# Kernel optimization log

Measured on AMD Instinct MI355X. Metric: run time of the kernel, lower is better.

## Reference

```python
import jax, jax.numpy as jnp
import numpy as np

N = 100000
E = 600000
D_IN, D_HID, D_OUT = 128, 128, 64


def setup_inputs() -> dict:
    key = jax.random.key(0)
    k1, k2, k3, k4 = jax.random.split(key, 4)
    x = jax.random.normal(k1, (N, D_IN), dtype=jnp.float32)
    edge_index = jax.random.randint(k2, (2, E), 0, N, dtype=jnp.int64)
    edge_weight = jnp.ones((E,), dtype=jnp.float32)
    W1 = jax.random.normal(k3, (D_IN, D_HID), dtype=jnp.float32) / np.sqrt(D_IN)
    b1 = jnp.zeros((D_HID,), dtype=jnp.float32)
    W2 = jax.random.normal(k4, (D_HID, D_OUT), dtype=jnp.float32) / np.sqrt(D_HID)
    b2 = jnp.zeros((D_OUT,), dtype=jnp.float32)
    return {"x": x, "edge_index": edge_index, "edge_weight": edge_weight,
            "W1": W1, "b1": b1, "W2": W2, "b2": b2}


def _gcn_conv(x, row, col, ew, W, b, n_nodes):
    # x: [N, d_in]; row/col/ew include self loops. PyG gcn_norm:
    # deg[i] = sum of ew over edges with target i; norm = d^-1/2[row]*ew*d^-1/2[col]
    deg = jax.ops.segment_sum(ew, col, num_segments=n_nodes)
    dinv = jnp.where(deg > 0, jax.lax.rsqrt(deg), 0.0)
    norm = dinv[row] * ew * dinv[col]  # [E+N]
    xw = x @ W  # dense transform first (d_out <= d_in path)
    msg = xw[row] * norm[:, None]  # gather + scale  [E+N, d_out]
    out = jax.ops.segment_sum(msg, col, num_segments=n_nodes)  # scatter-add
    return out + b


def reference(x, edge_index, edge_weight, W1, b1, W2, b2):
    n = x.shape[0]
    loops = jnp.arange(n, dtype=edge_index.dtype)
    row = jnp.concatenate([edge_index[0], loops])
    col = jnp.concatenate([edge_index[1], loops])
    ew = jnp.concatenate([edge_weight, jnp.ones((n,), dtype=edge_weight.dtype)])
    # dropout is identity in eval mode
    h = jax.nn.relu(_gcn_conv(x, row, col, ew, W1, b1, n))
    out = _gcn_conv(h, row, col, ew, W2, b2, n)
    return out
```

## Files before the change

kernel.cpp:

```cpp
#include <hip/hip_runtime.h>


constexpr int SCAN_BLOCKS = 256;

typedef __attribute__((ext_vector_type(8))) short short8;
typedef __attribute__((ext_vector_type(4))) float f32x4;

__device__ __forceinline__ ushort f2bf(float f) {
    unsigned u = __float_as_uint(f);
    return (ushort)((u + 0x7fffu + ((u >> 16) & 1u)) >> 16);
}
__device__ __forceinline__ float bf2f(ushort h) {
    return __uint_as_float((unsigned)h << 16);
}

__global__ void cnt_kernel(const int* __restrict__ col, int* __restrict__ cnt,
                           int* __restrict__ rank, int E) {
    const int stride = gridDim.x * blockDim.x;
    for (int e = blockIdx.x * blockDim.x + threadIdx.x; e < E; e += stride)
        rank[e] = atomicAdd(&cnt[col[e]], 1);
}

__global__ __launch_bounds__(256) void scan_part_kernel(
        const int* __restrict__ cnt, int* __restrict__ partial, int N) {
    const int T = SCAN_BLOCKS * 256;
    const int chunk = (N + T - 1) / T;
    const int j = blockIdx.x * 256 + threadIdx.x;
    const int s = j * chunk, e = min(s + chunk, N);
    int acc = 0;
    for (int i = s; i < e; i++) acc += cnt[i];
    __shared__ int red[256];
    red[threadIdx.x] = acc;
    __syncthreads();
    for (int off = 128; off > 0; off >>= 1) {
        if (threadIdx.x < off) red[threadIdx.x] += red[threadIdx.x + off];
        __syncthreads();
    }
    if (threadIdx.x == 0) partial[blockIdx.x] = red[0];
}

__global__ __launch_bounds__(256) void scan_tops_kernel(int* __restrict__ partial) {
    __shared__ int sh[256];
    const int t = threadIdx.x;
    int v = (t < SCAN_BLOCKS) ? partial[t] : 0;
    sh[t] = v;
    __syncthreads();
    for (int off = 1; off < 256; off <<= 1) {
        int x = sh[t];
        int a = (t >= off) ? sh[t - off] : 0;
        __syncthreads();
        sh[t] = x + a;
        __syncthreads();
    }
    if (t < SCAN_BLOCKS) partial[t] = (t == 0) ? 0 : sh[t - 1];
}

__global__ __launch_bounds__(256) void scan_write_kernel(
        const int* __restrict__ cnt, const int* __restrict__ partial,
        int* __restrict__ rowptr, int N) {
    const int T = SCAN_BLOCKS * 256;
    const int chunk = (N + T - 1) / T;
    const int j = blockIdx.x * 256 + threadIdx.x;
    const int s = j * chunk, e = min(s + chunk, N);
    int acc = 0;
    for (int i = s; i < e; i++) acc += cnt[i];
    __shared__ int sh[256];
    const int t = threadIdx.x;
    sh[t] = acc;
    __syncthreads();
    for (int off = 1; off < 256; off <<= 1) {
        int x = sh[t];
        int a = (t >= off) ? sh[t - off] : 0;
        __syncthreads();
        sh[t] = x + a;
        __syncthreads();
    }
    int excl = partial[blockIdx.x] + ((t == 0) ? 0 : sh[t - 1]);
    for (int i = s; i < e; i++) {
        rowptr[i] = excl;
        excl += cnt[i];
    }
    if (j == T - 1) rowptr[N] = excl;
}

__global__ void fill_kernel(const int* __restrict__ row, const int* __restrict__ col,
        const float* __restrict__ ew, const int* __restrict__ rowptr,
        const int* __restrict__ rank, int2* __restrict__ csr, int E) {
    int e = blockIdx.x * blockDim.x + threadIdx.x;
    if (e < E) {
        const int p = rowptr[col[e]] + rank[e];
        csr[p] = make_int2(row[e], __float_as_int(ew[e]));
    }
}

__global__ __launch_bounds__(256) void degsum_kernel(
        const int* __restrict__ rowptr, const int2* __restrict__ csr,
        float* __restrict__ dinv, int N) {
    const int n = blockIdx.x * blockDim.x + threadIdx.x;
    if (n >= N) return;
    const int e0 = rowptr[n], e1 = rowptr[n + 1];
    float d = 1.0f;
    for (int e = e0; e < e1; e++) d += __int_as_float(csr[e].y);
    dinv[n] = (d > 0.0f) ? rsqrtf(d) : 0.0f;
}

__global__ __launch_bounds__(256) void misc_kernel(
        int2* __restrict__ csr, const float* __restrict__ dinv, int E,
        const float* __restrict__ X, ushort* __restrict__ Xb, int nx4,
        const float* __restrict__ W1, ushort* __restrict__ W1t,
        const float* __restrict__ W2, ushort* __restrict__ W2t) {
    const int nb_x = (nx4 + 255) / 256;
    const int nb_p = (E + 255) / 256;
    int b = blockIdx.x;
    if (b < nb_x) {
        const int i = b * 256 + threadIdx.x;
        if (i < nx4) {
            float4 v = reinterpret_cast<const float4*>(X)[i];
            ushort4 o;
            o.x = f2bf(v.x); o.y = f2bf(v.y); o.z = f2bf(v.z); o.w = f2bf(v.w);
            reinterpret_cast<ushort4*>(Xb)[i] = o;
        }
        return;
    }
    b -= nb_x;
    if (b < nb_p) {
        const int e = b * 256 + threadIdx.x;
        if (e < E) {
            int2 c = csr[e];
            ((float*)csr)[2 * (size_t)e + 1] = __int_as_float(c.y) * dinv[c.x];
        }
        return;
    }
    b -= nb_p;
    if (b < 64) {
        const int o = b * 256 + threadIdx.x;
        W1t[o] = f2bf(W1[(size_t)(o & 127) * 128 + (o >> 7)]);
        return;
    }
    b -= 64;
    {
        const int o = b * 256 + threadIdx.x;
        if (o < 64 * 128)
            W2t[o] = f2bf(W2[(size_t)(o & 127) * 64 + (o >> 7)]);
    }
}

template <int DOUT, bool OUT_BF16>
__global__ __launch_bounds__(256, 2) void mfma_gemm_kernel(
        const ushort* __restrict__ Xb, const ushort* __restrict__ Wt,
        void* __restrict__ Y, int N) {
    constexpr int CW = DOUT / 64;
    constexpr int RW = 4 / CW;
    constexpr int WROWS = 128 / RW;
    constexpr int MI = WROWS / 16;
    __shared__ __align__(16) ushort sX[128 * 128];
    __shared__ __align__(16) ushort sW[DOUT * 128];
    const int tid = threadIdx.x;
    const int base = blockIdx.x * 128;

    #pragma unroll
    for (int p = 0; p < 8; p++) {
        const int ch = p * 256 + tid;
        const int r = ch >> 4, cpos = ch & 15;
        const int grow = base + r;
        uint4 v = make_uint4(0, 0, 0, 0);
        if (grow < N)
            v = *reinterpret_cast<const uint4*>(Xb + (size_t)grow * 128 + cpos * 8);
        const int b = (cpos * 16) ^ ((r & 7) << 4);
        *reinterpret_cast<uint4*>(reinterpret_cast<char*>(sX) + r * 256 + b) = v;
    }
    for (int ch = tid; ch < DOUT * 16; ch += 256) {
        const int r = ch >> 4, cpos = ch & 15;
        uint4 v = *reinterpret_cast<const uint4*>(Wt + (size_t)r * 128 + cpos * 8);
        const int b = (cpos * 16) ^ ((r & 7) << 4);
        *reinterpret_cast<uint4*>(reinterpret_cast<char*>(sW) + r * 256 + b) = v;
    }
    __syncthreads();

    const int lane = tid & 63;
    const int wid = tid >> 6;
    const int wr = wid / CW;
    const int wc = wid % CW;
    const int lr = lane & 15;
    const int g  = lane >> 4;

    f32x4 acc[MI][4];
    #pragma unroll
    for (int i = 0; i < MI; i++)
        #pragma unroll
        for (int f = 0; f < 4; f++)
            acc[i][f] = (f32x4){0.f, 0.f, 0.f, 0.f};

    #pragma unroll
    for (int ks = 0; ks < 4; ks++) {
        const int koff = ks * 64 + g * 16;
        short8 a[MI], b[4];
        #pragma unroll
        for (int i = 0; i < MI; i++) {
            const int row = wr * WROWS + i * 16 + lr;
            a[i] = *reinterpret_cast<const short8*>(
                reinterpret_cast<const char*>(sX) + row * 256 + (koff ^ ((row & 7) << 4)));
        }
        #pragma unroll
        for (int f = 0; f < 4; f++) {
            const int col = wc * 64 + f * 16 + lr;
            b[f] = *reinterpret_cast<const short8*>(
                reinterpret_cast<const char*>(sW) + col * 256 + (koff ^ ((col & 7) << 4)));
        }
        #pragma unroll
        for (int i = 0; i < MI; i++)
            #pragma unroll
            for (int f = 0; f < 4; f++)
                acc[i][f] = __builtin_amdgcn_mfma_f32_16x16x32_bf16(a[i], b[f], acc[i][f], 0, 0, 0);
    }

    #pragma unroll
    for (int i = 0; i < MI; i++) {
        #pragma unroll
        for (int reg = 0; reg < 4; reg++) {
            const int grow = base + wr * WROWS + i * 16 + g * 4 + reg;
            if (grow < N) {
                #pragma unroll
                for (int f = 0; f < 4; f++) {
                    const int gcol = wc * 64 + f * 16 + lr;
                    const float v = acc[i][f][reg];
                    if (OUT_BF16)
                        ((ushort*)Y)[(size_t)grow * DOUT + gcol] = f2bf(v);
                    else
                        ((float*)Y)[(size_t)grow * DOUT + gcol] = v;
                }
            }
        }
    }
}

__global__ __launch_bounds__(256) void agg1_kernel(
        const int* __restrict__ rowptr, const int2* __restrict__ csr,
        const float* __restrict__ dinv,
        const ushort* __restrict__ src, const float* __restrict__ bias,
        ushort* __restrict__ dst, int N) {
    const long long gid = (long long)blockIdx.x * blockDim.x + threadIdx.x;
    const int c = (int)(gid >> 5);
    if (c >= N) return;
    const int lane = (int)(gid & 31);
    const float di = dinv[c];
    const float sl = di * di;
    ushort4 s4 = *reinterpret_cast<const ushort4*>(src + (size_t)c * 128 + lane * 4);
    float ax = bf2f(s4.x) * sl, ay = bf2f(s4.y) * sl,
          az = bf2f(s4.z) * sl, aw = bf2f(s4.w) * sl;
    const int e0 = rowptr[c], e1 = rowptr[c + 1];
    int e = e0;
    for (; e + 4 <= e1; e += 4) {
        const int2 c0 = csr[e], c1 = csr[e + 1], c2 = csr[e + 2], c3 = csr[e + 3];
        const ushort4 v0 = *reinterpret_cast<const ushort4*>(src + (size_t)c0.x * 128 + lane * 4);
        const ushort4 v1 = *reinterpret_cast<const ushort4*>(src + (size_t)c1.x * 128 + lane * 4);
        const ushort4 v2 = *reinterpret_cast<const ushort4*>(src + (size_t)c2.x * 128 + lane * 4);
        const ushort4 v3 = *reinterpret_cast<const ushort4*>(src + (size_t)c3.x * 128 + lane * 4);
        const float w0 = __int_as_float(c0.y) * di;
        const float w1 = __int_as_float(c1.y) * di;
        const float w2 = __int_as_float(c2.y) * di;
        const float w3 = __int_as_float(c3.y) * di;
        ax += bf2f(v0.x) * w0 + bf2f(v1.x) * w1 + bf2f(v2.x) * w2 + bf2f(v3.x) * w3;
        ay += bf2f(v0.y) * w0 + bf2f(v1.y) * w1 + bf2f(v2.y) * w2 + bf2f(v3.y) * w3;
        az += bf2f(v0.z) * w0 + bf2f(v1.z) * w1 + bf2f(v2.z) * w2 + bf2f(v3.z) * w3;
        aw += bf2f(v0.w) * w0 + bf2f(v1.w) * w1 + bf2f(v2.w) * w2 + bf2f(v3.w) * w3;
    }
    for (; e < e1; e++) {
        const int2 ce = csr[e];
        const float w = __int_as_float(ce.y) * di;
        const ushort4 v4 = *reinterpret_cast<const ushort4*>(src + (size_t)ce.x * 128 + lane * 4);
        ax += bf2f(v4.x) * w; ay += bf2f(v4.y) * w;
        az += bf2f(v4.z) * w; aw += bf2f(v4.w) * w;
    }
    const float4 b = reinterpret_cast<const float4*>(bias)[lane];
    ax = fmaxf(ax + b.x, 0.f); ay = fmaxf(ay + b.y, 0.f);
    az = fmaxf(az + b.z, 0.f); aw = fmaxf(aw + b.w, 0.f);
    ushort4 o;
    o.x = f2bf(ax); o.y = f2bf(ay); o.z = f2bf(az); o.w = f2bf(aw);
    *reinterpret_cast<ushort4*>(dst + (size_t)c * 128 + lane * 4) = o;
}

__global__ __launch_bounds__(256) void agg2_kernel(
        const int* __restrict__ rowptr, const int2* __restrict__ csr,
        const float* __restrict__ dinv,
        const ushort* __restrict__ src, const float* __restrict__ bias,
        float* __restrict__ dst, int N) {
    const long long gid = (long long)blockIdx.x * blockDim.x + threadIdx.x;
    const int c = (int)(gid >> 4);
    if (c >= N) return;
    const int lane = (int)(gid & 15);
    const float di = dinv[c];
    const float sl = di * di;
    ushort4 s4 = *reinterpret_cast<const ushort4*>(src + (size_t)c * 64 + lane * 4);
    float ax = bf2f(s4.x) * sl, ay = bf2f(s4.y) * sl,
          az = bf2f(s4.z) * sl, aw = bf2f(s4.w) * sl;
    const int e0 = rowptr[c], e1 = rowptr[c + 1];
    int e = e0;
    for (; e + 4 <= e1; e += 4) {
        const int2 c0 = csr[e], c1 = csr[e + 1], c2 = csr[e + 2], c3 = csr[e + 3];
        const ushort4 v0 = *reinterpret_cast<const ushort4*>(src + (size_t)c0.x * 64 + lane * 4);
        const ushort4 v1 = *reinterpret_cast<const ushort4*>(src + (size_t)c1.x * 64 + lane * 4);
        const ushort4 v2 = *reinterpret_cast<const ushort4*>(src + (size_t)c2.x * 64 + lane * 4);
        const ushort4 v3 = *reinterpret_cast<const ushort4*>(src + (size_t)c3.x * 64 + lane * 4);
        const float w0 = __int_as_float(c0.y) * di;
        const float w1 = __int_as_float(c1.y) * di;
        const float w2 = __int_as_float(c2.y) * di;
        const float w3 = __int_as_float(c3.y) * di;
        ax += bf2f(v0.x) * w0 + bf2f(v1.x) * w1 + bf2f(v2.x) * w2 + bf2f(v3.x) * w3;
        ay += bf2f(v0.y) * w0 + bf2f(v1.y) * w1 + bf2f(v2.y) * w2 + bf2f(v3.y) * w3;
        az += bf2f(v0.z) * w0 + bf2f(v1.z) * w1 + bf2f(v2.z) * w2 + bf2f(v3.z) * w3;
        aw += bf2f(v0.w) * w0 + bf2f(v1.w) * w1 + bf2f(v2.w) * w2 + bf2f(v3.w) * w3;
    }
    for (; e < e1; e++) {
        const int2 ce = csr[e];
        const float w = __int_as_float(ce.y) * di;
        const ushort4 v4 = *reinterpret_cast<const ushort4*>(src + (size_t)ce.x * 64 + lane * 4);
        ax += bf2f(v4.x) * w; ay += bf2f(v4.y) * w;
        az += bf2f(v4.z) * w; aw += bf2f(v4.w) * w;
    }
    const float4 b = reinterpret_cast<const float4*>(bias)[lane];
    float4 o = make_float4(ax + b.x, ay + b.y, az + b.z, aw + b.w);
    reinterpret_cast<float4*>(dst)[(size_t)c * 16 + lane] = o;
}

extern "C" void kernel_launch(void* const* d_in, const int* in_sizes, int n_in,
                              void* d_out, int out_size, void* d_ws, size_t ws_size,
                              hipStream_t stream) {
    const float* x  = (const float*)d_in[0];
    const int*   ei = (const int*)d_in[1];
    const float* ew = (const float*)d_in[2];
    const float* W1 = (const float*)d_in[3];
    const float* b1 = (const float*)d_in[4];
    const float* W2 = (const float*)d_in[5];
    const float* b2 = (const float*)d_in[6];
    const int N = in_sizes[0] / 128;
    const int E = in_sizes[1] / 2;
    const int* row = ei;
    const int* col = ei + E;

    char* w = (char*)d_ws;
    float* dinv = (float*)w;                 w += (size_t)N * 4;
    ushort* Xb  = (ushort*)w;
    ushort* Gb  = (ushort*)w;
                                             w += (size_t)N * 256;
    ushort* Ab  = (ushort*)w;                w += (size_t)N * 256;
    ushort* Hb  = (ushort*)w;                w += (size_t)N * 256;
    ushort* W1t = (ushort*)w;                w += 128 * 128 * 2;
    ushort* W2t = (ushort*)w;                w += 64 * 128 * 2;
    int* cnt    = (int*)w;                   w += (size_t)N * 4;
    int* rowptr = (int*)w;                   w += (size_t)(N + 1) * 4;
    int* partial= (int*)w;                   w += SCAN_BLOCKS * 4;
    int* rank   = (int*)w;                   w += (size_t)E * 4;
    int2* csr   = (int2*)w;
    float* out  = (float*)d_out;

    hipMemsetAsync(cnt, 0, (size_t)N * sizeof(int), stream);

    const int eb4 = (E / 4 + 255) / 256;
    cnt_kernel<<<eb4, 256, 0, stream>>>(col, cnt, rank, E);
    scan_part_kernel<<<SCAN_BLOCKS, 256, 0, stream>>>(cnt, partial, N);
    scan_tops_kernel<<<1, 256, 0, stream>>>(partial);
    scan_write_kernel<<<SCAN_BLOCKS, 256, 0, stream>>>(cnt, partial, rowptr, N);
    fill_kernel<<<(E + 255) / 256, 256, 0, stream>>>(row, col, ew, rowptr, rank, csr, E);
    degsum_kernel<<<(N + 255) / 256, 256, 0, stream>>>(rowptr, csr, dinv, N);

    const int nx4 = N * 32;
    const int misc_blocks = (nx4 + 255) / 256 + (E + 255) / 256 + 64 + 32;
    misc_kernel<<<misc_blocks, 256, 0, stream>>>(csr, dinv, E, x, Xb, nx4,
                                                 W1, W1t, W2, W2t);

    const int ntiles = (N + 127) / 128;

    mfma_gemm_kernel<128, true><<<ntiles, 256, 0, stream>>>(Xb, W1t, Ab, N);
    agg1_kernel<<<(int)(((long long)N * 32 + 255) / 256), 256, 0, stream>>>(
        rowptr, csr, dinv, Ab, b1, Hb, N);

    mfma_gemm_kernel<64, true><<<ntiles, 256, 0, stream>>>(Hb, W2t, Gb, N);
    agg2_kernel<<<(int)(((long long)N * 16 + 255) / 256), 256, 0, stream>>>(
        rowptr, csr, dinv, Gb, b2, out, N);
}
```

Before: 161.3 us.

## Fuse X conversion into GEMM1, overlap edge counting, merge scan stages, widen aggregation

GEMM1 now reads fp32 X and converts it to bf16 while staging into shared memory, so the separate Xb pass is gone. Extra blocks in the same launch perform the atomic edge counting, overlapping that work with the GEMM. The memset is replaced by a prep kernel that also transposes the weights. The scan-tops kernel is folded into scan_write, and the per-edge dinv pre-scaling pass is dropped in favour of looking up dinv[src] inside the aggregation kernels. Aggregation now uses 16-byte loads with 8 features per thread, at the cost of an extra dependent gather per edge.

```diff
diff --git a/kernel.cpp b/kernel.cpp
--- a/kernel.cpp
+++ b/kernel.cpp
@@ -14,11 +14,123 @@
     return __uint_as_float((unsigned)h << 16);
 }
 
-__global__ void cnt_kernel(const int* __restrict__ col, int* __restrict__ cnt,
-                           int* __restrict__ rank, int E) {
-    const int stride = gridDim.x * blockDim.x;
-    for (int e = blockIdx.x * blockDim.x + threadIdx.x; e < E; e += stride)
-        rank[e] = atomicAdd(&cnt[col[e]], 1);
+__global__ __launch_bounds__(256) void prep_kernel(
+        int* __restrict__ cnt, int N,
+        const float* __restrict__ W1, ushort* __restrict__ W1t,
+        const float* __restrict__ W2, ushort* __restrict__ W2t) {
+    const int n4c = (N + 3) >> 2;
+    const int nbz = (n4c + 255) / 256;
+    int b = blockIdx.x;
+    if (b < nbz) {
+        const int i = b * 256 + threadIdx.x;
+        if (i < n4c) reinterpret_cast<int4*>(cnt)[i] = make_int4(0, 0, 0, 0);
+        return;
+    }
+    b -= nbz;
+    if (b < 64) {
+        const int o = b * 256 + threadIdx.x;
+        W1t[o] = f2bf(W1[(size_t)(o & 127) * 128 + (o >> 7)]);
+        return;
+    }
+    b -= 64;
+    {
+        const int o = b * 256 + threadIdx.x;
+        if (o < 64 * 128)
+            W2t[o] = f2bf(W2[(size_t)(o & 127) * 64 + (o >> 7)]);
+    }
+}
+
+__global__ __launch_bounds__(256, 2) void combo1_kernel(
+        const float* __restrict__ X, const ushort* __restrict__ W1t,
+        ushort* __restrict__ Ab, int N, int G,
+        const int* __restrict__ col, int* __restrict__ cnt,
+        int* __restrict__ rank, int E) {
+    __shared__ __align__(16) ushort sX[128 * 128];
+    __shared__ __align__(16) ushort sW[128 * 128];
+    const int tid = threadIdx.x;
+
+    if (blockIdx.x >= G) {
+        const int T = (gridDim.x - G) * 256;
+        for (int e = (blockIdx.x - G) * 256 + tid; e < E; e += T)
+            rank[e] = atomicAdd(&cnt[col[e]], 1);
+        return;
+    }
+
+    const int base = blockIdx.x * 128;
+    #pragma unroll
+    for (int p = 0; p < 8; p++) {
+        const int ch = p * 256 + tid;
+        const int r = ch >> 4, cpos = ch & 15;
+        const int grow = base + r;
+        uint4 u = make_uint4(0, 0, 0, 0);
+        if (grow < N) {
+            const float* xp = X + (size_t)grow * 128 + cpos * 8;
+            const float4 a = *reinterpret_cast<const float4*>(xp);
+            const float4 c = *reinterpret_cast<const float4*>(xp + 4);
+            u.x = (uint)f2bf(a.x) | ((uint)f2bf(a.y) << 16);
+            u.y = (uint)f2bf(a.z) | ((uint)f2bf(a.w) << 16);
+            u.z = (uint)f2bf(c.x) | ((uint)f2bf(c.y) << 16);
+            u.w = (uint)f2bf(c.z) | ((uint)f2bf(c.w) << 16);
+        }
+        const int b = (cpos * 16) ^ ((r & 7) << 4);
+        *reinterpret_cast<uint4*>(reinterpret_cast<char*>(sX) + r * 256 + b) = u;
+    }
+    #pragma unroll
+    for (int p = 0; p < 8; p++) {
+        const int ch = p * 256 + tid;
+        const int r = ch >> 4, cpos = ch & 15;
+        uint4 v = *reinterpret_cast<const uint4*>(W1t + (size_t)r * 128 + cpos * 8);
+        const int b = (cpos * 16) ^ ((r & 7) << 4);
+        *reinterpret_cast<uint4*>(reinterpret_cast<char*>(sW) + r * 256 + b) = v;
+    }
+    __syncthreads();
+
+    const int lane = tid & 63;
+    const int wid = tid >> 6;
+    const int wr = wid >> 1;
+    const int wc = wid & 1;
+    const int lr = lane & 15;
+    const int g  = lane >> 4;
+
+    f32x4 acc[4][4];
+    #pragma unroll
+    for (int i = 0; i < 4; i++)
+        #pragma unroll
+        for (int f = 0; f < 4; f++) acc[i][f] = (f32x4){0.f, 0.f, 0.f, 0.f};
+
+    #pragma unroll
+    for (int ks = 0; ks < 4; ks++) {
+        const int koff = ks * 64 + g * 16;
+        short8 a[4], b[4];
+        #pragma unroll
+        for (int i = 0; i < 4; i++) {
+            const int row = wr * 64 + i * 16 + lr;
+            a[i] = *reinterpret_cast<const short8*>(
+                reinterpret_cast<const char*>(sX) + row * 256 + (koff ^ ((row & 7) << 4)));
+        }
+        #pragma unroll
+        for (int f = 0; f < 4; f++) {
+            const int c = wc * 64 + f * 16 + lr;
+            b[f] = *reinterpret_cast<const short8*>(
+                reinterpret_cast<const char*>(sW) + c * 256 + (koff ^ ((c & 7) << 4)));
+        }
+        #pragma unroll
+        for (int i = 0; i < 4; i++)
+            #pragma unroll
+            for (int f = 0; f < 4; f++)
+                acc[i][f] = __builtin_amdgcn_mfma_f32_16x16x32_bf16(a[i], b[f], acc[i][f], 0, 0, 0);
+    }
+
+    #pragma unroll
+    for (int i = 0; i < 4; i++)
+        #pragma unroll
+        for (int reg = 0; reg < 4; reg++) {
+            const int grow = base + wr * 64 + i * 16 + g * 4 + reg;
+            if (grow < N)
+                #pragma unroll
+                for (int f = 0; f < 4; f++)
+                    Ab[(size_t)grow * 128 + wc * 64 + f * 16 + lr] = f2bf(acc[i][f][reg]);
+        }
 }
 
 __global__ __launch_bounds__(256) void scan_part_kernel(
@@ -39,33 +151,29 @@
     if (threadIdx.x == 0) partial[blockIdx.x] = red[0];
 }
 
-__global__ __launch_bounds__(256) void scan_tops_kernel(int* __restrict__ partial) {
-    __shared__ int sh[256];
-    const int t = threadIdx.x;
-    int v = (t < SCAN_BLOCKS) ? partial[t] : 0;
-    sh[t] = v;
-    __syncthreads();
-    for (int off = 1; off < 256; off <<= 1) {
-        int x = sh[t];
-        int a = (t >= off) ? sh[t - off] : 0;
-        __syncthreads();
-        sh[t] = x + a;
-        __syncthreads();
-    }
-    if (t < SCAN_BLOCKS) partial[t] = (t == 0) ? 0 : sh[t - 1];
-}
-
 __global__ __launch_bounds__(256) void scan_write_kernel(
         const int* __restrict__ cnt, const int* __restrict__ partial,
         int* __restrict__ rowptr, int N) {
+    __shared__ int tp[256];
+    __shared__ int sh[256];
+    const int t = threadIdx.x;
+    tp[t] = partial[t];
+    __syncthreads();
+    for (int off = 1; off < 256; off <<= 1) {
+        int x = tp[t];
+        int a = (t >= off) ? tp[t - off] : 0;
+        __syncthreads();
+        tp[t] = x + a;
+        __syncthreads();
+    }
+    const int blockOff = (blockIdx.x == 0) ? 0 : tp[blockIdx.x - 1];
+
     const int T = SCAN_BLOCKS * 256;
     const int chunk = (N + T - 1) / T;
-    const int j = blockIdx.x * 256 + threadIdx.x;
+    const int j = blockIdx.x * 256 + t;
     const int s = j * chunk, e = min(s + chunk, N);
     int acc = 0;
     for (int i = s; i < e; i++) acc += cnt[i];
-    __shared__ int sh[256];
-    const int t = threadIdx.x;
     sh[t] = acc;
     __syncthreads();
     for (int off = 1; off < 256; off <<= 1) {
@@ -75,7 +183,7 @@
         sh[t] = x + a;
         __syncthreads();
     }
-    int excl = partial[blockIdx.x] + ((t == 0) ? 0 : sh[t - 1]);
+    int excl = blockOff + ((t == 0) ? 0 : sh[t - 1]);
     for (int i = s; i < e; i++) {
         rowptr[i] = excl;
         excl += cnt[i];
@@ -104,57 +212,116 @@
     dinv[n] = (d > 0.0f) ? rsqrtf(d) : 0.0f;
 }
 
-__global__ __launch_bounds__(256) void misc_kernel(
-        int2* __restrict__ csr, const float* __restrict__ dinv, int E,
-        const float* __restrict__ X, ushort* __restrict__ Xb, int nx4,
-        const float* __restrict__ W1, ushort* __restrict__ W1t,
-        const float* __restrict__ W2, ushort* __restrict__ W2t) {
-    const int nb_x = (nx4 + 255) / 256;
-    const int nb_p = (E + 255) / 256;
-    int b = blockIdx.x;
-    if (b < nb_x) {
-        const int i = b * 256 + threadIdx.x;
-        if (i < nx4) {
-            float4 v = reinterpret_cast<const float4*>(X)[i];
-            ushort4 o;
-            o.x = f2bf(v.x); o.y = f2bf(v.y); o.z = f2bf(v.z); o.w = f2bf(v.w);
-            reinterpret_cast<ushort4*>(Xb)[i] = o;
-        }
-        return;
-    }
-    b -= nb_x;
-    if (b < nb_p) {
-        const int e = b * 256 + threadIdx.x;
-        if (e < E) {
-            int2 c = csr[e];
-            ((float*)csr)[2 * (size_t)e + 1] = __int_as_float(c.y) * dinv[c.x];
-        }
-        return;
-    }
-    b -= nb_p;
-    if (b < 64) {
-        const int o = b * 256 + threadIdx.x;
-        W1t[o] = f2bf(W1[(size_t)(o & 127) * 128 + (o >> 7)]);
-        return;
-    }
-    b -= 64;
+__global__ __launch_bounds__(256) void agg1_kernel(
+        const int* __restrict__ rowptr, const int2* __restrict__ csr,
+        const float* __restrict__ dinv,
+        const ushort* __restrict__ src, const float* __restrict__ bias,
+        ushort* __restrict__ dst, int N) {
+    const long long gid = (long long)blockIdx.x * blockDim.x + threadIdx.x;
+    const int c = (int)(gid >> 4);
+    if (c >= N) return;
+    const int lane = (int)(gid & 15);
+    const float di = dinv[c];
+    const float sl = di * di;
+    float acc[8];
     {
-        const int o = b * 256 + threadIdx.x;
-        if (o < 64 * 128)
-            W2t[o] = f2bf(W2[(size_t)(o & 127) * 64 + (o >> 7)]);
-    }
-}
-
-template <int DOUT, bool OUT_BF16>
-__global__ __launch_bounds__(256, 2) void mfma_gemm_kernel(
+        const short8 s8 = *reinterpret_cast<const short8*>(src + (size_t)c * 128 + lane * 8);
+        #pragma unroll
+        for (int j = 0; j < 8; j++) acc[j] = bf2f((ushort)s8[j]) * sl;
+    }
+    const int e0 = rowptr[c], e1 = rowptr[c + 1];
+    int e = e0;
+    for (; e + 4 <= e1; e += 4) {
+        const int2 c0 = csr[e], c1 = csr[e + 1], c2 = csr[e + 2], c3 = csr[e + 3];
+        const float w0 = __int_as_float(c0.y) * dinv[c0.x] * di;
+        const float w1 = __int_as_float(c1.y) * dinv[c1.x] * di;
+        const float w2 = __int_as_float(c2.y) * dinv[c2.x] * di;
+        const float w3 = __int_as_float(c3.y) * dinv[c3.x] * di;
+        const short8 v0 = *reinterpret_cast<const short8*>(src + (size_t)c0.x * 128 + lane * 8);
+        const short8 v1 = *reinterpret_cast<const short8*>(src + (size_t)c1.x * 128 + lane * 8);
+        const short8 v2 = *reinterpret_cast<const short8*>(src + (size_t)c2.x * 128 + lane * 8);
+        const short8 v3 = *reinterpret_cast<const short8*>(src + (size_t)c3.x * 128 + lane * 8);
+        #pragma unroll
+        for (int j = 0; j < 8; j++)
+            acc[j] += bf2f((ushort)v0[j]) * w0 + bf2f((ushort)v1[j]) * w1 +
+                      bf2f((ushort)v2[j]) * w2 + bf2f((ushort)v3[j]) * w3;
+    }
+    for (; e < e1; e++) {
+        const int2 ce = csr[e];
+        const float w = __int_as_float(ce.y) * dinv[ce.x] * di;
+        const short8 v = *reinterpret_cast<const short8*>(src + (size_t)ce.x * 128 + lane * 8);
+        #pragma unroll
+        for (int j = 0; j < 8; j++) acc[j] += bf2f((ushort)v[j]) * w;
+    }
+    const float4 b0 = reinterpret_cast<const float4*>(bias)[lane * 2];
+    const float4 b1 = reinterpret_cast<const float4*>(bias)[lane * 2 + 1];
+    acc[0] = fmaxf(acc[0] + b0.x, 0.f); acc[1] = fmaxf(acc[1] + b0.y, 0.f);
+    acc[2] = fmaxf(acc[2] + b0.z, 0.f); acc[3] = fmaxf(acc[3] + b0.w, 0.f);
+    acc[4] = fmaxf(acc[4] + b1.x, 0.f); acc[5] = fmaxf(acc[5] + b1.y, 0.f);
+    acc[6] = fmaxf(acc[6] + b1.z, 0.f); acc[7] = fmaxf(acc[7] + b1.w, 0.f);
+    uint4 o;
+    o.x = (uint)f2bf(acc[0]) | ((uint)f2bf(acc[1]) << 16);
+    o.y = (uint)f2bf(acc[2]) | ((uint)f2bf(acc[3]) << 16);
+    o.z = (uint)f2bf(acc[4]) | ((uint)f2bf(acc[5]) << 16);
+    o.w = (uint)f2bf(acc[6]) | ((uint)f2bf(acc[7]) << 16);
+    *reinterpret_cast<uint4*>(dst + (size_t)c * 128 + lane * 8) = o;
+}
+
+__global__ __launch_bounds__(256) void agg2_kernel(
+        const int* __restrict__ rowptr, const int2* __restrict__ csr,
+        const float* __restrict__ dinv,
+        const ushort* __restrict__ src, const float* __restrict__ bias,
+        float* __restrict__ dst, int N) {
+    const long long gid = (long long)blockIdx.x * blockDim.x + threadIdx.x;
+    const int c = (int)(gid >> 3);
+    if (c >= N) return;
+    const int lane = (int)(gid & 7);
+    const float di = dinv[c];
+    const float sl = di * di;
+    float acc[8];
+    {
+        const short8 s8 = *reinterpret_cast<const short8*>(src + (size_t)c * 64 + lane * 8);
+        #pragma unroll
+        for (int j = 0; j < 8; j++) acc[j] = bf2f((ushort)s8[j]) * sl;
+    }
+    const int e0 = rowptr[c], e1 = rowptr[c + 1];
+    int e = e0;
+    for (; e + 4 <= e1; e += 4) {
+        const int2 c0 = csr[e], c1 = csr[e + 1], c2 = csr[e + 2], c3 = csr[e + 3];
+        const float w0 = __int_as_float(c0.y) * dinv[c0.x] * di;
+        const float w1 = __int_as_float(c1.y) * dinv[c1.x] * di;
+        const float w2 = __int_as_float(c2.y) * dinv[c2.x] * di;
+        const float w3 = __int_as_float(c3.y) * dinv[c3.x] * di;
+        const short8 v0 = *reinterpret_cast<const short8*>(src + (size_t)c0.x * 64 + lane * 8);
+        const short8 v1 = *reinterpret_cast<const short8*>(src + (size_t)c1.x * 64 + lane * 8);
+        const short8 v2 = *reinterpret_cast<const short8*>(src + (size_t)c2.x * 64 + lane * 8);
+        const short8 v3 = *reinterpret_cast<const short8*>(src + (size_t)c3.x * 64 + lane * 8);
+        #pragma unroll
+        for (int j = 0; j < 8; j++)
+            acc[j] += bf2f((ushort)v0[j]) * w0 + bf2f((ushort)v1[j]) * w1 +
+                      bf2f((ushort)v2[j]) * w2 + bf2f((ushort)v3[j]) * w3;
+    }
+    for (; e < e1; e++) {
+        const int2 ce = csr[e];
+        const float w = __int_as_float(ce.y) * dinv[ce.x] * di;
+        const short8 v = *reinterpret_cast<const short8*>(src + (size_t)ce.x * 64 + lane * 8);
+        #pragma unroll
+        for (int j = 0; j < 8; j++) acc[j] += bf2f((ushort)v[j]) * w;
+    }
+    const float4 b0 = reinterpret_cast<const float4*>(bias)[lane * 2];
+    const float4 b1 = reinterpret_cast<const float4*>(bias)[lane * 2 + 1];
+    float* dp = dst + (size_t)c * 64 + lane * 8;
+    *reinterpret_cast<float4*>(dp) =
+        make_float4(acc[0] + b0.x, acc[1] + b0.y, acc[2] + b0.z, acc[3] + b0.w);
+    *reinterpret_cast<float4*>(dp + 4) =
+        make_float4(acc[4] + b1.x, acc[5] + b1.y, acc[6] + b1.z, acc[7] + b1.w);
+}
+
+__global__ __launch_bounds__(256, 2) void gemm2_kernel(
         const ushort* __restrict__ Xb, const ushort* __restrict__ Wt,
-        void* __restrict__ Y, int N) {
-    constexpr int CW = DOUT / 64;
-    constexpr int RW = 4 / CW;
-    constexpr int WROWS = 128 / RW;
-    constexpr int MI = WROWS / 16;
+        ushort* __restrict__ Y, int N) {
     __shared__ __align__(16) ushort sX[128 * 128];
-    __shared__ __align__(16) ushort sW[DOUT * 128];
+    __shared__ __align__(16) ushort sW[64 * 128];
     const int tid = threadIdx.x;
     const int base = blockIdx.x * 128;
 
@@ -169,7 +336,9 @@
         const int b = (cpos * 16) ^ ((r & 7) << 4);
         *reinterpret_cast<uint4*>(reinterpret_cast<char*>(sX) + r * 256 + b) = v;
     }
-    for (int ch = tid; ch < DOUT * 16; ch += 256) {
+    #pragma unroll
+    for (int p = 0; p < 4; p++) {
+        const int ch = p * 256 + tid;
         const int r = ch >> 4, cpos = ch & 15;
         uint4 v = *reinterpret_cast<const uint4*>(Wt + (size_t)r * 128 + cpos * 8);
         const int b = (cpos * 16) ^ ((r & 7) << 4);
@@ -179,148 +348,48 @@
 
     const int lane = tid & 63;
     const int wid = tid >> 6;
-    const int wr = wid / CW;
-    const int wc = wid % CW;
     const int lr = lane & 15;
     const int g  = lane >> 4;
 
-    f32x4 acc[MI][4];
-    #pragma unroll
-    for (int i = 0; i < MI; i++)
-        #pragma unroll
-        for (int f = 0; f < 4; f++)
-            acc[i][f] = (f32x4){0.f, 0.f, 0.f, 0.f};
+    f32x4 acc[2][4];
+    #pragma unroll
+    for (int i = 0; i < 2; i++)
+        #pragma unroll
+        for (int f = 0; f < 4; f++) acc[i][f] = (f32x4){0.f, 0.f, 0.f, 0.f};
 
     #pragma unroll
     for (int ks = 0; ks < 4; ks++) {
         const int koff = ks * 64 + g * 16;
-        short8 a[MI], b[4];
-        #pragma unroll
-        for (int i = 0; i < MI; i++) {
-            const int row = wr * WROWS + i * 16 + lr;
+        short8 a[2], b[4];
+        #pragma unroll
+        for (int i = 0; i < 2; i++) {
+            const int row = wid * 32 + i * 16 + lr;
             a[i] = *reinterpret_cast<const short8*>(
                 reinterpret_cast<const char*>(sX) + row * 256 + (koff ^ ((row & 7) << 4)));
         }
         #pragma unroll
         for (int f = 0; f < 4; f++) {
-            const int col = wc * 64 + f * 16 + lr;
+            const int c = f * 16 + lr;
             b[f] = *reinterpret_cast<const short8*>(
-                reinterpret_cast<const char*>(sW) + col * 256 + (koff ^ ((col & 7) << 4)));
-        }
-        #pragma unroll
-        for (int i = 0; i < MI; i++)
+                reinterpret_cast<const char*>(sW) + c * 256 + (koff ^ ((c & 7) << 4)));
+        }
+        #pragma unroll
+        for (int i = 0; i < 2; i++)
             #pragma unroll
             for (int f = 0; f < 4; f++)
                 acc[i][f] = __builtin_amdgcn_mfma_f32_16x16x32_bf16(a[i], b[f], acc[i][f], 0, 0, 0);
     }
 
     #pragma unroll
-    for (int i = 0; i < MI; i++) {
+    for (int i = 0; i < 2; i++)
         #pragma unroll
         for (int reg = 0; reg < 4; reg++) {
-            const int grow = base + wr * WROWS + i * 16 + g * 4 + reg;
-            if (grow < N) {
+            const int grow = base + wid * 32 + i * 16 + g * 4 + reg;
+            if (grow < N)
                 #pragma unroll
-                for (int f = 0; f < 4; f++) {
-                    const int gcol = wc * 64 + f * 16 + lr;
-                    const float v = acc[i][f][reg];
-                    if (OUT_BF16)
-                        ((ushort*)Y)[(size_t)grow * DOUT + gcol] = f2bf(v);
-                    else
-                        ((float*)Y)[(size_t)grow * DOUT + gcol] = v;
-                }
-            }
-        }
-    }
-}
-
-__global__ __launch_bounds__(256) void agg1_kernel(
-        const int* __restrict__ rowptr, const int2* __restrict__ csr,
-        const float* __restrict__ dinv,
-        const ushort* __restrict__ src, const float* __restrict__ bias,
-        ushort* __restrict__ dst, int N) {
-    const long long gid = (long long)blockIdx.x * blockDim.x + threadIdx.x;
-    const int c = (int)(gid >> 5);
-    if (c >= N) return;
-    const int lane = (int)(gid & 31);
-    const float di = dinv[c];
-    const float sl = di * di;
-    ushort4 s4 = *reinterpret_cast<const ushort4*>(src + (size_t)c * 128 + lane * 4);
-    float ax = bf2f(s4.x) * sl, ay = bf2f(s4.y) * sl,
-          az = bf2f(s4.z) * sl, aw = bf2f(s4.w) * sl;
-    const int e0 = rowptr[c], e1 = rowptr[c + 1];
-    int e = e0;
-    for (; e + 4 <= e1; e += 4) {
-        const int2 c0 = csr[e], c1 = csr[e + 1], c2 = csr[e + 2], c3 = csr[e + 3];
-        const ushort4 v0 = *reinterpret_cast<const ushort4*>(src + (size_t)c0.x * 128 + lane * 4);
-        const ushort4 v1 = *reinterpret_cast<const ushort4*>(src + (size_t)c1.x * 128 + lane * 4);
-        const ushort4 v2 = *reinterpret_cast<const ushort4*>(src + (size_t)c2.x * 128 + lane * 4);
-        const ushort4 v3 = *reinterpret_cast<const ushort4*>(src + (size_t)c3.x * 128 + lane * 4);
-        const float w0 = __int_as_float(c0.y) * di;
-        const float w1 = __int_as_float(c1.y) * di;
-        const float w2 = __int_as_float(c2.y) * di;
-        const float w3 = __int_as_float(c3.y) * di;
-        ax += bf2f(v0.x) * w0 + bf2f(v1.x) * w1 + bf2f(v2.x) * w2 + bf2f(v3.x) * w3;
-        ay += bf2f(v0.y) * w0 + bf2f(v1.y) * w1 + bf2f(v2.y) * w2 + bf2f(v3.y) * w3;
-        az += bf2f(v0.z) * w0 + bf2f(v1.z) * w1 + bf2f(v2.z) * w2 + bf2f(v3.z) * w3;
-        aw += bf2f(v0.w) * w0 + bf2f(v1.w) * w1 + bf2f(v2.w) * w2 + bf2f(v3.w) * w3;
-    }
-    for (; e < e1; e++) {
-        const int2 ce = csr[e];
-        const float w = __int_as_float(ce.y) * di;
-        const ushort4 v4 = *reinterpret_cast<const ushort4*>(src + (size_t)ce.x * 128 + lane * 4);
-        ax += bf2f(v4.x) * w; ay += bf2f(v4.y) * w;
-        az += bf2f(v4.z) * w; aw += bf2f(v4.w) * w;
-    }
-    const float4 b = reinterpret_cast<const float4*>(bias)[lane];
-    ax = fmaxf(ax + b.x, 0.f); ay = fmaxf(ay + b.y, 0.f);
-    az = fmaxf(az + b.z, 0.f); aw = fmaxf(aw + b.w, 0.f);
-    ushort4 o;
-    o.x = f2bf(ax); o.y = f2bf(ay); o.z = f2bf(az); o.w = f2bf(aw);
-    *reinterpret_cast<ushort4*>(dst + (size_t)c * 128 + lane * 4) = o;
-}
-
-__global__ __launch_bounds__(256) void agg2_kernel(
-        const int* __restrict__ rowptr, const int2* __restrict__ csr,
-        const float* __restrict__ dinv,
-        const ushort* __restrict__ src, const float* __restrict__ bias,
-        float* __restrict__ dst, int N) {
-    const long long gid = (long long)blockIdx.x * blockDim.x + threadIdx.x;
-    const int c = (int)(gid >> 4);
-    if (c >= N) return;
-    const int lane = (int)(gid & 15);
-    const float di = dinv[c];
-    const float sl = di * di;
-    ushort4 s4 = *reinterpret_cast<const ushort4*>(src + (size_t)c * 64 + lane * 4);
-    float ax = bf2f(s4.x) * sl, ay = bf2f(s4.y) * sl,
-          az = bf2f(s4.z) * sl, aw = bf2f(s4.w) * sl;
-    const int e0 = rowptr[c], e1 = rowptr[c + 1];
-    int e = e0;
-    for (; e + 4 <= e1; e += 4) {
-        const int2 c0 = csr[e], c1 = csr[e + 1], c2 = csr[e + 2], c3 = csr[e + 3];
-        const ushort4 v0 = *reinterpret_cast<const ushort4*>(src + (size_t)c0.x * 64 + lane * 4);
-        const ushort4 v1 = *reinterpret_cast<const ushort4*>(src + (size_t)c1.x * 64 + lane * 4);
-        const ushort4 v2 = *reinterpret_cast<const ushort4*>(src + (size_t)c2.x * 64 + lane * 4);
-        const ushort4 v3 = *reinterpret_cast<const ushort4*>(src + (size_t)c3.x * 64 + lane * 4);
-        const float w0 = __int_as_float(c0.y) * di;
-        const float w1 = __int_as_float(c1.y) * di;
-        const float w2 = __int_as_float(c2.y) * di;
-        const float w3 = __int_as_float(c3.y) * di;
-        ax += bf2f(v0.x) * w0 + bf2f(v1.x) * w1 + bf2f(v2.x) * w2 + bf2f(v3.x) * w3;
-        ay += bf2f(v0.y) * w0 + bf2f(v1.y) * w1 + bf2f(v2.y) * w2 + bf2f(v3.y) * w3;
-        az += bf2f(v0.z) * w0 + bf2f(v1.z) * w1 + bf2f(v2.z) * w2 + bf2f(v3.z) * w3;
-        aw += bf2f(v0.w) * w0 + bf2f(v1.w) * w1 + bf2f(v2.w) * w2 + bf2f(v3.w) * w3;
-    }
-    for (; e < e1; e++) {
-        const int2 ce = csr[e];
-        const float w = __int_as_float(ce.y) * di;
-        const ushort4 v4 = *reinterpret_cast<const ushort4*>(src + (size_t)ce.x * 64 + lane * 4);
-        ax += bf2f(v4.x) * w; ay += bf2f(v4.y) * w;
-        az += bf2f(v4.z) * w; aw += bf2f(v4.w) * w;
-    }
-    const float4 b = reinterpret_cast<const float4*>(bias)[lane];
-    float4 o = make_float4(ax + b.x, ay + b.y, az + b.z, aw + b.w);
-    reinterpret_cast<float4*>(dst)[(size_t)c * 16 + lane] = o;
+                for (int f = 0; f < 4; f++)
+                    Y[(size_t)grow * 64 + f * 16 + lr] = f2bf(acc[i][f][reg]);
+        }
 }
 
 extern "C" void kernel_launch(void* const* d_in, const int* in_sizes, int n_in,
@@ -340,42 +409,36 @@
 
     char* w = (char*)d_ws;
     float* dinv = (float*)w;                 w += (size_t)N * 4;
-    ushort* Xb  = (ushort*)w;
-    ushort* Gb  = (ushort*)w;
-                                             w += (size_t)N * 256;
     ushort* Ab  = (ushort*)w;                w += (size_t)N * 256;
     ushort* Hb  = (ushort*)w;                w += (size_t)N * 256;
+    ushort* Gb  = (ushort*)w;                w += (size_t)N * 128;
     ushort* W1t = (ushort*)w;                w += 128 * 128 * 2;
     ushort* W2t = (ushort*)w;                w += 64 * 128 * 2;
-    int* cnt    = (int*)w;                   w += (size_t)N * 4;
+    int* cnt    = (int*)w;                   w += (size_t)N * 4 + 16;
     int* rowptr = (int*)w;                   w += (size_t)(N + 1) * 4;
     int* partial= (int*)w;                   w += SCAN_BLOCKS * 4;
     int* rank   = (int*)w;                   w += (size_t)E * 4;
     int2* csr   = (int2*)w;
     float* out  = (float*)d_out;
 
-    hipMemsetAsync(cnt, 0, (size_t)N * sizeof(int), stream);
-
-    const int eb4 = (E / 4 + 255) / 256;
-    cnt_kernel<<<eb4, 256, 0, stream>>>(col, cnt, rank, E);
+    const int ntiles = (N + 127) / 128;
+    const int nbz = (((N + 3) >> 2) + 255) / 256;
+
+    prep_kernel<<<nbz + 64 + 32, 256, 0, stream>>>(cnt, N, W1, W1t, W2, W2t);
+
+    const int cntb = (E / 4 + 255) / 256;
+    combo1_kernel<<<ntiles + cntb, 256, 0, stream>>>(x, W1t, Ab, N, ntiles,
+                                                     col, cnt, rank, E);
+
     scan_part_kernel<<<SCAN_BLOCKS, 256, 0, stream>>>(cnt, partial, N);
-    scan_tops_kernel<<<1, 256, 0, stream>>>(partial);
     scan_write_kernel<<<SCAN_BLOCKS, 256, 0, stream>>>(cnt, partial, rowptr, N);
     fill_kernel<<<(E + 255) / 256, 256, 0, stream>>>(row, col, ew, rowptr, rank, csr, E);
     degsum_kernel<<<(N + 255) / 256, 256, 0, stream>>>(rowptr, csr, dinv, N);
 
-    const int nx4 = N * 32;
-    const int misc_blocks = (nx4 + 255) / 256 + (E + 255) / 256 + 64 + 32;
-    misc_kernel<<<misc_blocks, 256, 0, stream>>>(csr, dinv, E, x, Xb, nx4,
-                                                 W1, W1t, W2, W2t);
-
-    const int ntiles = (N + 127) / 128;
-
-    mfma_gemm_kernel<128, true><<<ntiles, 256, 0, stream>>>(Xb, W1t, Ab, N);
-    agg1_kernel<<<(int)(((long long)N * 32 + 255) / 256), 256, 0, stream>>>(
+    agg1_kernel<<<(int)(((long long)N * 16 + 255) / 256), 256, 0, stream>>>(
         rowptr, csr, dinv, Ab, b1, Hb, N);
 
-    mfma_gemm_kernel<64, true><<<ntiles, 256, 0, stream>>>(Hb, W2t, Gb, N);
-    agg2_kernel<<<(int)(((long long)N * 16 + 255) / 256), 256, 0, stream>>>(
+    gemm2_kernel<<<ntiles, 256, 0, stream>>>(Hb, W2t, Gb, N);
+    agg2_kernel<<<(int)(((long long)N * 8 + 255) / 256), 256, 0, stream>>>(
         rowptr, csr, dinv, Gb, b2, out, N);
 }
```

Result: faster. 131.0 us (-18.8%).
